# Optimization experiments

Hardware: AMD Instinct MI355X
Metric: run time of the kernel (lower is better)

The kernel has to match this reference:

```python
import jax, jax.numpy as jnp
import numpy as np

RING_WORLD_SIZE = 4  # number of ring steps / KV sequence chunks


def _ring_flash_attention(q, k, v, ring_size):
    # q,k,v: [B, S, H, D]; non-causal full attention computed blockwise over
    # KV chunks (one per ring step) with numerically-stable online LSE merge,
    # mirroring _compact_ring_fwd + update_out_and_lse.
    B, S, H, D = q.shape
    scale = D ** (-0.5)
    chunk = S // ring_size
    out = None  # [B, S, H, D] accumulated in fp32
    lse = None  # [B, H, S] running log-sum-exp
    for step in range(ring_size):
        k_blk = jax.lax.dynamic_slice_in_dim(k, step * chunk, chunk, axis=1)
        v_blk = jax.lax.dynamic_slice_in_dim(v, step * chunk, chunk, axis=1)
        # scores: [B, H, Sq, Sk_blk]
        scores = jnp.einsum('bqhd,bkhd->bhqk', q, k_blk) * scale
        block_lse = jax.scipy.special.logsumexp(scores, axis=-1)  # [B,H,Sq]
        probs = jnp.exp(scores - block_lse[..., None])
        block_out = jnp.einsum('bhqk,bkhd->bqhd', probs, v_blk)
        if out is None:
            out, lse = block_out, block_lse
        else:
            new_lse = jnp.logaddexp(lse, block_lse)
            w_old = jnp.exp(lse - new_lse)       # [B,H,Sq]
            w_new = jnp.exp(block_lse - new_lse)
            # broadcast weights to [B,Sq,H,1]
            out = (jnp.transpose(w_old, (0, 2, 1))[..., None] * out
                   + jnp.transpose(w_new, (0, 2, 1))[..., None] * block_out)
            lse = new_lse
    return out.astype(q.dtype)


def setup_inputs() -> dict:
    key = jax.random.key(0)
    kq, kk, kv = jax.random.split(key, 3)
    shape = (1, 4096, 16, 128)
    return {
        'query': jax.random.normal(kq, shape, dtype=jnp.float32),
        'key': jax.random.normal(kk, shape, dtype=jnp.float32),
        'value': jax.random.normal(kv, shape, dtype=jnp.float32),
    }


def reference(query, key, value):
    # Ulysses all-to-all is identity on a single logical device; the ring loop
    # with lossless (error-feedback) KV compression reduces to blockwise
    # attention with online softmax merging.
    return _ring_flash_attention(query, key, value, RING_WORLD_SIZE)
```

## Files before the change

### kernel.cpp

```cpp
#include <hip/hip_runtime.h>
#include <hip/hip_bf16.h>

#define S_LEN 4096
#define NH    16
#define DD    128
#define HD    2048
#define QB    128
#define KB    64
#define NT    (S_LEN/KB)

typedef __bf16 bf16_t;
typedef bf16_t bf16x8 __attribute__((ext_vector_type(8)));
typedef bf16_t bf16x4 __attribute__((ext_vector_type(4)));
typedef float  f32x4  __attribute__((ext_vector_type(4)));

static __device__ __forceinline__ bf16x8 pack8(float4 a, float4 b, float s) {
  bf16x8 v;
  v[0]=(bf16_t)(a.x*s); v[1]=(bf16_t)(a.y*s); v[2]=(bf16_t)(a.z*s); v[3]=(bf16_t)(a.w*s);
  v[4]=(bf16_t)(b.x*s); v[5]=(bf16_t)(b.y*s); v[6]=(bf16_t)(b.z*s); v[7]=(bf16_t)(b.w*s);
  return v;
}

static __device__ __forceinline__ void gload_lds16(const void* g, void* l) {
  __builtin_amdgcn_global_load_lds((const __attribute__((address_space(1))) void*)g,
                                   (__attribute__((address_space(3))) void*)l, 16, 0, 0);
}

__global__ __launch_bounds__(256) void prep_k(const float* __restrict__ Kg,
                                              bf16_t* __restrict__ Kp) {
  int idx = blockIdx.x * 256 + threadIdx.x;
  int jp = idx & 15;
  int s  = (idx >> 4) & (S_LEN - 1);
  int h  = idx >> 16;
  int jl = jp ^ (s & 7);
  const float* src = Kg + (size_t)s*HD + h*DD + jl*8;
  float4 a = *(const float4*)src;
  float4 b = *(const float4*)(src + 4);
  *(bf16x8*)(Kp + ((size_t)h*S_LEN + s)*DD + jp*8) = pack8(a, b, 1.0f);
}

__global__ __launch_bounds__(256) void prep_v(const float* __restrict__ Vg,
                                              bf16_t* __restrict__ Vp) {
  int kt = blockIdx.x;
  int h  = blockIdx.y;
  int tid = threadIdx.x;
  __shared__ bf16_t tile[KB][DD + 8];
  #pragma unroll
  for (int it = 0; it < 8; ++it) {
    int lin4 = it*256 + tid;
    int r  = lin4 >> 5;
    int dc = (lin4 & 31) * 4;
    float4 a = *(const float4*)(Vg + (size_t)(kt*KB + r)*HD + h*DD + dc);
    tile[r][dc+0]=(bf16_t)a.x; tile[r][dc+1]=(bf16_t)a.y;
    tile[r][dc+2]=(bf16_t)a.z; tile[r][dc+3]=(bf16_t)a.w;
  }
  __syncthreads();
  bf16_t* out = Vp + (size_t)(h*NT + kt)*DD*KB;
  #pragma unroll
  for (int it = 0; it < 4; ++it) {
    int cid = it*256 + tid;
    int d  = cid >> 3;
    int jp = cid & 7;
    bf16x8 v;
    #pragma unroll
    for (int m = 0; m < 8; ++m) {
      int c = ((jp ^ (d & 7)) << 3) + m;
      int k = 32*(c>>5) + 16*((c>>2)&1) + 4*((c>>3)&3) + (c&3);
      v[m] = tile[k][d];
    }
    *(bf16x8*)(out + d*KB + jp*8) = v;
  }
}

__global__ __launch_bounds__(256, 2) void attn_fwd(const float* __restrict__ Qg,
                                                   const bf16_t* __restrict__ Kp,
                                                   const bf16_t* __restrict__ Vp,
                                                   float* __restrict__ Og) {
  const int phys = blockIdx.x;
  const int logical = (phys & 7) * 64 + (phys >> 3);
  const int h  = logical >> 5;
  const int qt = logical & 31;
  const int tid  = threadIdx.x;
  const int wid  = tid >> 6;
  const int lane = tid & 63;
  const int l16  = lane & 15;
  const int lg   = lane >> 4;

  __shared__ alignas(16) bf16_t Ks[2][KB*DD];
  __shared__ alignas(16) bf16_t Vt[2][DD*KB];

  const float qs = 0.08838834764831845f * 1.4426950408889634f;
  bf16x8 qf[2][4];
  #pragma unroll
  for (int g = 0; g < 2; ++g) {
    const int qrow = qt*QB + wid*32 + g*16 + l16;
    const float* qp = Qg + (size_t)qrow*HD + h*DD + lg*8;
    #pragma unroll
    for (int c = 0; c < 4; ++c) {
      float4 a = *(const float4*)(qp + c*32);
      float4 b = *(const float4*)(qp + c*32 + 4);
      qf[g][c] = pack8(a, b, qs);
    }
  }
  bf16x8 onesf;
  #pragma unroll
  for (int j = 0; j < 8; ++j) onesf[j] = (bf16_t)1.0f;
  asm volatile("" ::: "memory");

  const int lo = tid*16;
  auto issue = [&](int kt) {
    int b = kt & 1;
    const char* kg = (const char*)(Kp + ((size_t)h*S_LEN + kt*KB)*DD);
    const char* vg = (const char*)(Vp + (size_t)(h*NT + kt)*DD*KB);
    char* kl = (char*)&Ks[b][0];
    char* vl = (char*)&Vt[b][0];
    #pragma unroll
    for (int p = 0; p < 4; ++p) gload_lds16(kg + lo + p*4096, kl + lo + p*4096);
    #pragma unroll
    for (int p = 0; p < 4; ++p) gload_lds16(vg + lo + p*4096, vl + lo + p*4096);
  };

  f32x4 acc[2][8];
  f32x4 acc_l[2];
  #pragma unroll
  for (int g = 0; g < 2; ++g) {
    #pragma unroll
    for (int i = 0; i < 8; ++i) acc[g][i] = (f32x4){0.f,0.f,0.f,0.f};
    acc_l[g] = (f32x4){0.f,0.f,0.f,0.f};
  }
  float m_run[2] = {-__builtin_inff(), -__builtin_inff()};

  issue(0);
  issue(1);

  for (int kt = 0; kt < NT; ++kt) {
    if (kt == NT-1) { asm volatile("s_waitcnt vmcnt(0)" ::: "memory"); }
    else            { asm volatile("s_waitcnt vmcnt(8)" ::: "memory"); }
    __builtin_amdgcn_s_barrier();
    asm volatile("" ::: "memory");

    const int cur = kt & 1;
    const char* KsB = (const char*)&Ks[cur][0];
    const char* VtB = (const char*)&Vt[cur][0];

    f32x4 sc[2][4];
    #pragma unroll
    for (int g = 0; g < 2; ++g)
      #pragma unroll
      for (int b = 0; b < 4; ++b) sc[g][b] = (f32x4){0.f,0.f,0.f,0.f};
    __builtin_amdgcn_s_setprio(1);
    #pragma unroll
    for (int b = 0; b < 4; ++b) {
      int row = b*16 + l16;
      int rs  = row*256;
      int sw  = (row & 7) << 4;
      #pragma unroll
      for (int c = 0; c < 4; ++c) {
        int d0 = c*32 + lg*8;
        bf16x8 kb = *(const bf16x8*)(KsB + rs + ((d0*2) ^ sw));
        sc[0][b] = __builtin_amdgcn_mfma_f32_16x16x32_bf16(kb, qf[0][c], sc[0][b], 0, 0, 0);
        sc[1][b] = __builtin_amdgcn_mfma_f32_16x16x32_bf16(kb, qf[1][c], sc[1][b], 0, 0, 0);
      }
    }
    __builtin_amdgcn_s_setprio(0);

    bf16x4 pb[2][4];
    #pragma unroll
    for (int g = 0; g < 2; ++g) {
      float pmax;
      {
        float t0 = fmaxf(fmaxf(sc[g][0][0], sc[g][0][1]), fmaxf(sc[g][0][2], sc[g][0][3]));
        float t1 = fmaxf(fmaxf(sc[g][1][0], sc[g][1][1]), fmaxf(sc[g][1][2], sc[g][1][3]));
        float t2 = fmaxf(fmaxf(sc[g][2][0], sc[g][2][1]), fmaxf(sc[g][2][2], sc[g][2][3]));
        float t3 = fmaxf(fmaxf(sc[g][3][0], sc[g][3][1]), fmaxf(sc[g][3][2], sc[g][3][3]));
        pmax = fmaxf(fmaxf(t0, t1), fmaxf(t2, t3));
        pmax = fmaxf(pmax, __shfl_xor(pmax, 16));
        pmax = fmaxf(pmax, __shfl_xor(pmax, 32));
      }
      if (!__all(pmax - m_run[g] <= 8.0f)) {
        float mnew  = fmaxf(m_run[g], pmax);
        float alpha = exp2f(m_run[g] - mnew);
        m_run[g] = mnew;
        #pragma unroll
        for (int i = 0; i < 8; ++i) {
          #pragma unroll
          for (int r = 0; r < 4; ++r) acc[g][i][r] *= alpha;
        }
        #pragma unroll
        for (int r = 0; r < 4; ++r) acc_l[g][r] *= alpha;
      }
      #pragma unroll
      for (int b = 0; b < 4; ++b) {
        #pragma unroll
        for (int r = 0; r < 4; ++r) {
          float p = exp2f(sc[g][b][r] - m_run[g]);
          pb[g][b][r] = (bf16_t)p;
        }
      }
    }

    __builtin_amdgcn_s_setprio(1);
    #pragma unroll
    for (int ks = 0; ks < 2; ++ks) {
      bf16x8 pp0, pp1;
      #pragma unroll
      for (int j = 0; j < 4; ++j) {
        pp0[j] = pb[0][2*ks][j]; pp0[4+j] = pb[0][2*ks+1][j];
        pp1[j] = pb[1][2*ks][j]; pp1[4+j] = pb[1][2*ks+1][j];
      }
      acc_l[0] = __builtin_amdgcn_mfma_f32_16x16x32_bf16(onesf, pp0, acc_l[0], 0, 0, 0);
      acc_l[1] = __builtin_amdgcn_mfma_f32_16x16x32_bf16(onesf, pp1, acc_l[1], 0, 0, 0);
      #pragma unroll
      for (int db = 0; db < 8; ++db) {
        int d = db*16 + l16;
        bf16x8 va = *(const bf16x8*)(VtB + d*128 + ((64*ks + lg*16) ^ ((d & 7) << 4)));
        acc[0][db] = __builtin_amdgcn_mfma_f32_16x16x32_bf16(va, pp0, acc[0][db], 0, 0, 0);
        acc[1][db] = __builtin_amdgcn_mfma_f32_16x16x32_bf16(va, pp1, acc[1][db], 0, 0, 0);
      }
    }
    __builtin_amdgcn_s_setprio(0);

    __builtin_amdgcn_s_barrier();
    asm volatile("" ::: "memory");
    if (kt + 2 < NT) issue(kt + 2);
  }

  #pragma unroll
  for (int g = 0; g < 2; ++g) {
    const int qrow = qt*QB + wid*32 + g*16 + l16;
    const float inv = 1.0f / acc_l[g][0];
    float* op = Og + (size_t)qrow*HD + h*DD + lg*4;
    #pragma unroll
    for (int db = 0; db < 8; ++db) {
      float4 o;
      o.x = acc[g][db][0]*inv; o.y = acc[g][db][1]*inv;
      o.z = acc[g][db][2]*inv; o.w = acc[g][db][3]*inv;
      *(float4*)(op + db*16) = o;
    }
  }
}

extern "C" void kernel_launch(void* const* d_in, const int* in_sizes, int n_in,
                              void* d_out, int out_size, void* d_ws, size_t ws_size,
                              hipStream_t stream) {
  const float* Q = (const float*)d_in[0];
  const float* K = (const float*)d_in[1];
  const float* V = (const float*)d_in[2];
  float* O = (float*)d_out;
  bf16_t* Kp = (bf16_t*)d_ws;
  bf16_t* Vp = Kp + (size_t)NH*S_LEN*DD;
  prep_k<<<dim3(NH*S_LEN*16/256), 256, 0, stream>>>(K, Kp);
  prep_v<<<dim3(NT, NH), 256, 0, stream>>>(V, Vp);
  attn_fwd<<<dim3(512), 256, 0, stream>>>(Q, Kp, Vp, O);
}
```

Measured before the change: 198.9 us.

## Pre-permute K and V tiles into MFMA fragment order for linear LDS reads

```diff
diff --git a/kernel.cpp b/kernel.cpp
--- a/kernel.cpp
+++ b/kernel.cpp
@@ -11,7 +11,6 @@
 
 typedef __bf16 bf16_t;
 typedef bf16_t bf16x8 __attribute__((ext_vector_type(8)));
-typedef bf16_t bf16x4 __attribute__((ext_vector_type(4)));
 typedef float  f32x4  __attribute__((ext_vector_type(4)));
 
 static __device__ __forceinline__ bf16x8 pack8(float4 a, float4 b, float s) {
@@ -28,22 +27,34 @@
 
 __global__ __launch_bounds__(256) void prep_k(const float* __restrict__ Kg,
                                               bf16_t* __restrict__ Kp) {
-  int idx = blockIdx.x * 256 + threadIdx.x;
-  int jp = idx & 15;
-  int s  = (idx >> 4) & (S_LEN - 1);
-  int h  = idx >> 16;
-  int jl = jp ^ (s & 7);
-  const float* src = Kg + (size_t)s*HD + h*DD + jl*8;
-  float4 a = *(const float4*)src;
-  float4 b = *(const float4*)(src + 4);
-  *(bf16x8*)(Kp + ((size_t)h*S_LEN + s)*DD + jp*8) = pack8(a, b, 1.0f);
+  const int kt = blockIdx.x, h = blockIdx.y, tid = threadIdx.x;
+  __shared__ bf16_t tile[KB][DD + 8];
+  #pragma unroll
+  for (int it = 0; it < 8; ++it) {
+    int lin4 = it*256 + tid;
+    int r  = lin4 >> 5;
+    int dc = (lin4 & 31) * 4;
+    float4 a = *(const float4*)(Kg + (size_t)(kt*KB + r)*HD + h*DD + dc);
+    tile[r][dc+0]=(bf16_t)a.x; tile[r][dc+1]=(bf16_t)a.y;
+    tile[r][dc+2]=(bf16_t)a.z; tile[r][dc+3]=(bf16_t)a.w;
+  }
+  __syncthreads();
+  bf16_t* out = Kp + (size_t)(h*NT + kt)*8192;
+  #pragma unroll
+  for (int it = 0; it < 4; ++it) {
+    int cid = it*256 + tid;
+    int f = cid >> 6, l = cid & 63;
+    int b = f >> 2, c = f & 3;
+    int row = b*16 + (l & 15);
+    int d0  = c*32 + (l >> 4)*8;
+    bf16x8 v = *(const bf16x8*)(&tile[row][d0]);
+    *(bf16x8*)(out + (size_t)cid*8) = v;
+  }
 }
 
 __global__ __launch_bounds__(256) void prep_v(const float* __restrict__ Vg,
                                               bf16_t* __restrict__ Vp) {
-  int kt = blockIdx.x;
-  int h  = blockIdx.y;
-  int tid = threadIdx.x;
+  const int kt = blockIdx.x, h = blockIdx.y, tid = threadIdx.x;
   __shared__ bf16_t tile[KB][DD + 8];
   #pragma unroll
   for (int it = 0; it < 8; ++it) {
@@ -55,20 +66,22 @@
     tile[r][dc+2]=(bf16_t)a.z; tile[r][dc+3]=(bf16_t)a.w;
   }
   __syncthreads();
-  bf16_t* out = Vp + (size_t)(h*NT + kt)*DD*KB;
+  bf16_t* out = Vp + (size_t)(h*NT + kt)*8192;
   #pragma unroll
   for (int it = 0; it < 4; ++it) {
     int cid = it*256 + tid;
-    int d  = cid >> 3;
-    int jp = cid & 7;
+    int f = cid >> 6, l = cid & 63;
+    int ks = f >> 3, db = f & 7;
+    int d  = db*16 + (l & 15);
+    int c0 = ks*32 + (l >> 4)*8;
     bf16x8 v;
     #pragma unroll
     for (int m = 0; m < 8; ++m) {
-      int c = ((jp ^ (d & 7)) << 3) + m;
+      int c = c0 + m;
       int k = 32*(c>>5) + 16*((c>>2)&1) + 4*((c>>3)&3) + (c&3);
       v[m] = tile[k][d];
     }
-    *(bf16x8*)(out + d*KB + jp*8) = v;
+    *(bf16x8*)(out + (size_t)cid*8) = v;
   }
 }
 
@@ -85,9 +98,10 @@
   const int lane = tid & 63;
   const int l16  = lane & 15;
   const int lg   = lane >> 4;
-
-  __shared__ alignas(16) bf16_t Ks[2][KB*DD];
-  __shared__ alignas(16) bf16_t Vt[2][DD*KB];
+  const int lo16 = lane * 16;
+
+  __shared__ alignas(16) bf16_t Ks[2][8192];
+  __shared__ alignas(16) bf16_t Vt[2][8192];
 
   const float qs = 0.08838834764831845f * 1.4426950408889634f;
   bf16x8 qf[2][4];
@@ -110,8 +124,8 @@
   const int lo = tid*16;
   auto issue = [&](int kt) {
     int b = kt & 1;
-    const char* kg = (const char*)(Kp + ((size_t)h*S_LEN + kt*KB)*DD);
-    const char* vg = (const char*)(Vp + (size_t)(h*NT + kt)*DD*KB);
+    const char* kg = (const char*)(Kp + (size_t)(h*NT + kt)*8192);
+    const char* vg = (const char*)(Vp + (size_t)(h*NT + kt)*8192);
     char* kl = (char*)&Ks[b][0];
     char* vl = (char*)&Vt[b][0];
     #pragma unroll
@@ -140,8 +154,8 @@
     asm volatile("" ::: "memory");
 
     const int cur = kt & 1;
-    const char* KsB = (const char*)&Ks[cur][0];
-    const char* VtB = (const char*)&Vt[cur][0];
+    const char* KsB = (const char*)&Ks[cur][0] + lo16;
+    const char* VtB = (const char*)&Vt[cur][0] + lo16;
 
     f32x4 sc[2][4];
     #pragma unroll
@@ -151,29 +165,34 @@
     __builtin_amdgcn_s_setprio(1);
     #pragma unroll
     for (int b = 0; b < 4; ++b) {
-      int row = b*16 + l16;
-      int rs  = row*256;
-      int sw  = (row & 7) << 4;
       #pragma unroll
       for (int c = 0; c < 4; ++c) {
-        int d0 = c*32 + lg*8;
-        bf16x8 kb = *(const bf16x8*)(KsB + rs + ((d0*2) ^ sw));
+        bf16x8 kb = *(const bf16x8*)(KsB + ((b*4 + c) << 10));
         sc[0][b] = __builtin_amdgcn_mfma_f32_16x16x32_bf16(kb, qf[0][c], sc[0][b], 0, 0, 0);
         sc[1][b] = __builtin_amdgcn_mfma_f32_16x16x32_bf16(kb, qf[1][c], sc[1][b], 0, 0, 0);
       }
     }
     __builtin_amdgcn_s_setprio(0);
 
-    bf16x4 pb[2][4];
+    bf16x8 vf0[8], vf1[8];
+    #pragma unroll
+    for (int db = 0; db < 8; ++db) vf0[db] = *(const bf16x8*)(VtB + (db << 10));
+    #pragma unroll
+    for (int db = 0; db < 8; ++db) vf1[db] = *(const bf16x8*)(VtB + ((8 + db) << 10));
+
+    bf16x8 pp[2][2];
     #pragma unroll
     for (int g = 0; g < 2; ++g) {
       float pmax;
       {
-        float t0 = fmaxf(fmaxf(sc[g][0][0], sc[g][0][1]), fmaxf(sc[g][0][2], sc[g][0][3]));
-        float t1 = fmaxf(fmaxf(sc[g][1][0], sc[g][1][1]), fmaxf(sc[g][1][2], sc[g][1][3]));
-        float t2 = fmaxf(fmaxf(sc[g][2][0], sc[g][2][1]), fmaxf(sc[g][2][2], sc[g][2][3]));
-        float t3 = fmaxf(fmaxf(sc[g][3][0], sc[g][3][1]), fmaxf(sc[g][3][2], sc[g][3][3]));
-        pmax = fmaxf(fmaxf(t0, t1), fmaxf(t2, t3));
+        float a0 = fmaxf(fmaxf(sc[g][0][0], sc[g][0][1]), sc[g][0][2]);
+        float a1 = fmaxf(fmaxf(sc[g][0][3], sc[g][1][0]), sc[g][1][1]);
+        float a2 = fmaxf(fmaxf(sc[g][1][2], sc[g][1][3]), sc[g][2][0]);
+        float a3 = fmaxf(fmaxf(sc[g][2][1], sc[g][2][2]), sc[g][2][3]);
+        float a4 = fmaxf(fmaxf(sc[g][3][0], sc[g][3][1]), sc[g][3][2]);
+        float b0 = fmaxf(fmaxf(a0, a1), a2);
+        float b1 = fmaxf(fmaxf(a3, a4), sc[g][3][3]);
+        pmax = fmaxf(b0, b1);
         pmax = fmaxf(pmax, __shfl_xor(pmax, 16));
         pmax = fmaxf(pmax, __shfl_xor(pmax, 32));
       }
@@ -194,7 +213,7 @@
         #pragma unroll
         for (int r = 0; r < 4; ++r) {
           float p = exp2f(sc[g][b][r] - m_run[g]);
-          pb[g][b][r] = (bf16_t)p;
+          pp[g][b >> 1][(b & 1)*4 + r] = (bf16_t)p;
         }
       }
     }
@@ -202,20 +221,13 @@
     __builtin_amdgcn_s_setprio(1);
     #pragma unroll
     for (int ks = 0; ks < 2; ++ks) {
-      bf16x8 pp0, pp1;
-      #pragma unroll
-      for (int j = 0; j < 4; ++j) {
-        pp0[j] = pb[0][2*ks][j]; pp0[4+j] = pb[0][2*ks+1][j];
-        pp1[j] = pb[1][2*ks][j]; pp1[4+j] = pb[1][2*ks+1][j];
-      }
-      acc_l[0] = __builtin_amdgcn_mfma_f32_16x16x32_bf16(onesf, pp0, acc_l[0], 0, 0, 0);
-      acc_l[1] = __builtin_amdgcn_mfma_f32_16x16x32_bf16(onesf, pp1, acc_l[1], 0, 0, 0);
+      acc_l[0] = __builtin_amdgcn_mfma_f32_16x16x32_bf16(onesf, pp[0][ks], acc_l[0], 0, 0, 0);
+      acc_l[1] = __builtin_amdgcn_mfma_f32_16x16x32_bf16(onesf, pp[1][ks], acc_l[1], 0, 0, 0);
       #pragma unroll
       for (int db = 0; db < 8; ++db) {
-        int d = db*16 + l16;
-        bf16x8 va = *(const bf16x8*)(VtB + d*128 + ((64*ks + lg*16) ^ ((d & 7) << 4)));
-        acc[0][db] = __builtin_amdgcn_mfma_f32_16x16x32_bf16(va, pp0, acc[0][db], 0, 0, 0);
-        acc[1][db] = __builtin_amdgcn_mfma_f32_16x16x32_bf16(va, pp1, acc[1][db], 0, 0, 0);
+        bf16x8 va = ks ? vf1[db] : vf0[db];
+        acc[0][db] = __builtin_amdgcn_mfma_f32_16x16x32_bf16(va, pp[0][ks], acc[0][db], 0, 0, 0);
+        acc[1][db] = __builtin_amdgcn_mfma_f32_16x16x32_bf16(va, pp[1][ks], acc[1][db], 0, 0, 0);
       }
     }
     __builtin_amdgcn_s_setprio(0);
@@ -249,7 +261,7 @@
   float* O = (float*)d_out;
   bf16_t* Kp = (bf16_t*)d_ws;
   bf16_t* Vp = Kp + (size_t)NH*S_LEN*DD;
-  prep_k<<<dim3(NH*S_LEN*16/256), 256, 0, stream>>>(K, Kp);
+  prep_k<<<dim3(NT, NH), 256, 0, stream>>>(K, Kp);
   prep_v<<<dim3(NT, NH), 256, 0, stream>>>(V, Vp);
   attn_fwd<<<dim3(512), 256, 0, stream>>>(Q, Kp, Vp, O);
 }
```

Result: faster. 188.4 us (-5.3%).
